# Optimization experiments

Hardware: AMD Instinct MI355X
Metric: run time of the kernel (lower is better)

Reference implementation:

```python
import jax, jax.numpy as jnp
import numpy as np

SCALES = (128.0, 256.0, 512.0)
ASPECT = (0.5, 1.0, 2.0)
K = 9
NMS_THR = 0.7
PRE_NMS_TOPK = 10000
POST_NMS_TOPK = 2000
MIN_SIZE = 16.0

def conv2d(x, w, b, pad):
    out = jax.lax.conv_general_dilated(x, w, (1, 1), [(pad, pad), (pad, pad)], dimension_numbers=('NCHW', 'OIHW', 'NCHW'))
    return out + b[None, :, None, None]

def generate_anchors(grid_h, grid_w, dtype):
    # Faithful to source: shifts are grid indices, NOT multiplied by stride (source bug kept).
    scales = jnp.asarray(SCALES, dtype)
    ar = jnp.asarray(ASPECT, dtype)
    h_ratio = jnp.sqrt(ar)
    w_ratio = 1.0 / h_ratio
    ws = (w_ratio[:, None] * scales[None, :]).reshape(-1)
    hs = (h_ratio[:, None] * scales[None, :]).reshape(-1)
    base = jnp.round(jnp.stack([-ws, -hs, ws, hs], axis=1) / 2.0)  # (9,4)
    sy, sx = jnp.meshgrid(jnp.arange(grid_h), jnp.arange(grid_w), indexing='ij')
    sx = sx.reshape(-1).astype(dtype)
    sy = sy.reshape(-1).astype(dtype)
    shifts = jnp.stack([sx, sy, sx, sy], axis=1)  # (H*W,4)
    return (shifts[:, None, :] + base[None, :, :]).reshape(-1, 4)  # (H*W*9,4)

def decode(box_pred, anchors):
    w = anchors[:, 2] - anchors[:, 0]
    h = anchors[:, 3] - anchors[:, 1]
    cx = anchors[:, 0] + 0.5 * w
    cy = anchors[:, 1] + 0.5 * h
    dx, dy, dw, dh = box_pred[:, 0], box_pred[:, 1], box_pred[:, 2], box_pred[:, 3]
    pcx = dx * w + cx
    pcy = dy * h + cy
    pw = jnp.exp(dw) * w
    ph = jnp.exp(dh) * h
    return jnp.stack([pcx - 0.5 * pw, pcy - 0.5 * ph, pcx + 0.5 * pw, pcy + 0.5 * ph], axis=1)

def nms_keep(boxes, valid, thr):
    # Greedy NMS on score-descending boxes; invalid (small) boxes never kept nor suppress others.
    n = boxes.shape[0]
    x1, y1, x2, y2 = boxes[:, 0], boxes[:, 1], boxes[:, 2], boxes[:, 3]
    areas = (x2 - x1) * (y2 - y1)
    idx = jnp.arange(n)
    def body(i, keep):
        xx1 = jnp.maximum(x1, x1[i]); yy1 = jnp.maximum(y1, y1[i])
        xx2 = jnp.minimum(x2, x2[i]); yy2 = jnp.minimum(y2, y2[i])
        inter = jnp.maximum(xx2 - xx1, 0.0) * jnp.maximum(yy2 - yy1, 0.0)
        iou = inter / (areas + areas[i] - inter)
        suppress = (iou > thr) & (idx > i) & keep[i]
        return keep & (~suppress)
    return jax.lax.fori_loop(0, n, body, valid)

def filter_proposals(proposals, cls_scores, img_h, img_w):
    scores = jax.nn.sigmoid(cls_scores.reshape(-1))
    top_scores, top_idx = jax.lax.top_k(scores, PRE_NMS_TOPK)  # sorted descending
    props = proposals[top_idx]
    x1 = jnp.clip(props[:, 0], 0.0, img_w); y1 = jnp.clip(props[:, 1], 0.0, img_h)
    x2 = jnp.clip(props[:, 2], 0.0, img_w); y2 = jnp.clip(props[:, 3], 0.0, img_h)
    props = jnp.stack([x1, y1, x2, y2], axis=1)
    valid = ((x2 - x1) >= MIN_SIZE) & ((y2 - y1) >= MIN_SIZE)
    keep = jax.lax.stop_gradient(nms_keep(jax.lax.stop_gradient(props), valid, NMS_THR))
    masked = jnp.where(keep, top_scores, -1.0)
    final_scores, final_idx = jax.lax.top_k(masked, POST_NMS_TOPK)  # order = score-descending (matches post-NMS sort)
    final_props = props[final_idx]
    valid_out = final_scores > 0.0  # sigmoid scores > 0, padding = -1
    return jnp.where(valid_out[:, None], final_props, 0.0), jnp.where(valid_out, final_scores, 0.0)

def setup_inputs():
    key = jax.random.key(0)
    ks = jax.random.split(key, 8)
    C = 512; GH = GW = 50
    feat = jax.random.normal(ks[0], (1, C, GH, GW), jnp.float32)
    image = jnp.zeros((1, 3, 800, 800), jnp.float32)
    gt_boxes = jax.random.uniform(ks[1], (8, 4), jnp.float32) * 800.0
    w_rpn = jax.random.normal(ks[2], (C, C, 3, 3), jnp.float32) * 0.01
    b_rpn = jnp.zeros((C,), jnp.float32)
    w_cls = jax.random.normal(ks[3], (K, C, 1, 1), jnp.float32) * 0.01
    b_cls = jnp.zeros((K,), jnp.float32)
    w_reg = jax.random.normal(ks[4], (4 * K, C, 1, 1), jnp.float32) * 0.01
    b_reg = jnp.zeros((4 * K,), jnp.float32)
    return {"image": image, "feat": feat, "gt_boxes": gt_boxes, "w_rpn": w_rpn, "b_rpn": b_rpn, "w_cls": w_cls, "b_cls": b_cls, "w_reg": w_reg, "b_reg": b_reg}

def reference(image, feat, gt_boxes, w_rpn, b_rpn, w_cls, b_cls, w_reg, b_reg):
    rpn_feat = jax.nn.relu(conv2d(feat, w_rpn, b_rpn, 1))
    cls = conv2d(rpn_feat, w_cls, b_cls, 0)      # (B,9,H,W)
    reg = conv2d(rpn_feat, w_reg, b_reg, 0)      # (B,36,H,W)
    B, _, gh, gw = feat.shape
    anchors = generate_anchors(gh, gw, feat.dtype)
    # flatten to anchor ordering (h, w, k) matching generate_anchors
    cls_flat = jnp.transpose(cls, (0, 2, 3, 1)).reshape(-1)
    reg_flat = jnp.transpose(reg.reshape(B, K, 4, gh, gw), (0, 3, 4, 1, 2)).reshape(-1, 4)
    proposals = decode(reg_flat, anchors)
    img_h, img_w = float(image.shape[-2]), float(image.shape[-1])
    return filter_proposals(proposals, cls_flat, img_h, img_w)
```

## Files before the change

### kernel.cpp

```cpp
#include <hip/hip_runtime.h>
#include <cmath>
#include <cstdint>
#include <cstddef>

typedef unsigned long long u64;
typedef unsigned int u32;

#define NPX   2500
#define NANCH 22500
#define PRE_TOPK 10000
#define NWORDS 160

struct AnchorBase { float b[36]; };

typedef __attribute__((ext_vector_type(8))) short bf16x8;
typedef __attribute__((ext_vector_type(4))) float f32x4;

__device__ inline unsigned short f2bf(float f) {
    u32 u = __float_as_uint(f);
    u32 r = u + 0x7fffu + ((u >> 16) & 1u);
    return (unsigned short)(r >> 16);
}
__device__ inline float bf2f(unsigned short h) {
    return __uint_as_float(((u32)h) << 16);
}

__global__ __launch_bounds__(256) void kprep(const float* __restrict__ feat,
                                             const float* __restrict__ wr,
                                             unsigned short* __restrict__ xthi,
                                             unsigned short* __restrict__ xtlo,
                                             unsigned short* __restrict__ whi,
                                             unsigned short* __restrict__ wlo)
{
    __shared__ float sh[4608];
    int bid = blockIdx.x;
    int t = threadIdx.x;
    if (bid < 416) {
        float (*tile)[65] = (float(*)[65])sh;
        int gr = bid >> 3;
        int cc = bid & 7;
        int tx = t & 63, ty = t >> 6;
        int y = gr - 1;
        bool rowok = (gr >= 1) && (gr <= 50);
#pragma unroll
        for (int i = 0; i < 16; ++i) {
            int c = i * 4 + ty;
            tile[c][tx] = (rowok && tx < 50)
                        ? feat[(size_t)(cc * 64 + c) * NPX + y * 50 + tx] : 0.f;
        }
        __syncthreads();
#pragma unroll
        for (int i = 0; i < 16; ++i) {
            int xp = i * 4 + ty;
            int cell = gr * 64 + xp;
            bool ok = rowok && xp >= 1 && xp <= 50;
            float v = ok ? tile[tx][xp - 1] : 0.f;
            unsigned short hi = f2bf(v);
            xthi[(size_t)cell * 512 + cc * 64 + tx] = hi;
            xtlo[(size_t)cell * 512 + cc * 64 + tx] = f2bf(v - bf2f(hi));
        }
    } else {
        int oc = bid - 416;
        for (int j = t; j < 4608; j += 256) sh[j] = wr[(size_t)oc * 4608 + j];
        __syncthreads();
        for (int k = t; k < 4608; k += 256) {
            int c = k & 511, tap = k >> 9;
            float v = sh[c * 9 + tap];
            unsigned short hi = f2bf(v);
            whi[(size_t)oc * 4608 + k] = hi;
            wlo[(size_t)oc * 4608 + k] = f2bf(v - bf2f(hi));
        }
    }
}

__global__ __launch_bounds__(256) void k1m(const unsigned short* __restrict__ xthi,
                                           const unsigned short* __restrict__ xtlo,
                                           const unsigned short* __restrict__ whi,
                                           const unsigned short* __restrict__ wlo,
                                           float* __restrict__ pk,
                                           int cptLog, int cptm1, int cptMul, int niter)
{
    __shared__ __align__(16) unsigned short Ah[8192];
    __shared__ __align__(16) unsigned short Al[8192];
    __shared__ __align__(16) unsigned short Bh[8192];
    __shared__ __align__(16) unsigned short Bl[8192];

    int t = threadIdx.x;
    int lane = t & 63, wave = t >> 6;
    int wo = wave & 1, wp = wave >> 1;
    int ocb = blockIdx.x, pxb = blockIdx.y, bs = blockIdx.z;
    int q = lane >> 4, m = lane & 15;
    int c0base = bs * cptMul;

    int g  = t & 7;
    int r0 = t >> 3;
    int cellB[4];
    int ocA[4];
#pragma unroll
    for (int i = 0; i < 4; ++i) {
        int rl = r0 + 32 * i;
        int opx = pxb * 128 + rl;
        cellB[i] = (opx < NPX) ? ((opx / 50) + 1) * 64 + (opx % 50) + 1 : 190;
        ocA[i] = ocb * 128 + rl;
    }

    f32x4 acc[16];
    f32x4 zf = {0.f, 0.f, 0.f, 0.f};
#pragma unroll
    for (int i = 0; i < 16; ++i) acc[i] = zf;

    for (int it = 0; it < niter; ++it) {
        int tap = it >> cptLog;
        int cw  = it & cptm1;
        int c0  = c0base + cw * 64;
        int t3  = (tap * 43) >> 7;
        int tapoff = (t3 - 1) * 64 + (tap - t3 * 3) - 1;
#pragma unroll
        for (int i = 0; i < 4; ++i) {
            int rl = r0 + 32 * i;
            int la = rl * 64 + g * 8;
            size_t ga = (size_t)ocA[i] * 4608 + tap * 512 + c0 + g * 8;
            *(bf16x8*)(Ah + la) = *(const bf16x8*)(whi + ga);
            *(bf16x8*)(Al + la) = *(const bf16x8*)(wlo + ga);
            size_t gb = (size_t)(cellB[i] + tapoff) * 512 + c0 + g * 8;
            *(bf16x8*)(Bh + la) = *(const bf16x8*)(xthi + gb);
            *(bf16x8*)(Bl + la) = *(const bf16x8*)(xtlo + gb);
        }
        __syncthreads();
#pragma unroll
        for (int ks = 0; ks < 2; ++ks) {
            bf16x8 fah[4], fal[4], fbh[4], fbl[4];
#pragma unroll
            for (int mt = 0; mt < 4; ++mt) {
                int off = (wo * 64 + mt * 16 + m) * 64 + ks * 32 + q * 8;
                fah[mt] = *(const bf16x8*)(Ah + off);
                fal[mt] = *(const bf16x8*)(Al + off);
            }
#pragma unroll
            for (int nt = 0; nt < 4; ++nt) {
                int off = (wp * 64 + nt * 16 + m) * 64 + ks * 32 + q * 8;
                fbh[nt] = *(const bf16x8*)(Bh + off);
                fbl[nt] = *(const bf16x8*)(Bl + off);
            }
#pragma unroll
            for (int mt = 0; mt < 4; ++mt)
#pragma unroll
                for (int nt = 0; nt < 4; ++nt) {
                    f32x4 a = acc[mt * 4 + nt];
                    a = __builtin_amdgcn_mfma_f32_16x16x32_bf16(fal[mt], fbh[nt], a, 0, 0, 0);
                    a = __builtin_amdgcn_mfma_f32_16x16x32_bf16(fah[mt], fbl[nt], a, 0, 0, 0);
                    a = __builtin_amdgcn_mfma_f32_16x16x32_bf16(fah[mt], fbh[nt], a, 0, 0, 0);
                    acc[mt * 4 + nt] = a;
                }
        }
        __syncthreads();
    }
#pragma unroll
    for (int mt = 0; mt < 4; ++mt)
#pragma unroll
        for (int nt = 0; nt < 4; ++nt)
#pragma unroll
            for (int r = 0; r < 4; ++r) {
                int oc = ocb * 128 + wo * 64 + mt * 16 + q * 4 + r;
                int px = pxb * 128 + wp * 64 + nt * 16 + m;
                pk[((size_t)bs * 512 + oc) * 2560 + px] = acc[mt * 4 + nt][r];
            }
}

__global__ __launch_bounds__(256) void k2a_heads(const float* __restrict__ pk, int ns,
                                                 const float* __restrict__ br,
                                                 const float* __restrict__ wcls,
                                                 const float* __restrict__ wreg,
                                                 float* __restrict__ part)
{
    __shared__ float vt[64 * 64];
    __shared__ float Wl[45 * 64];
    int t  = threadIdx.x;
    int pb = blockIdx.x;
    int s  = blockIdx.y;
    int cb = s * 64;
    for (int e = t; e < 45 * 64; e += 256) {
        int u = e >> 6, c = e & 63;
        Wl[e] = (u < 9) ? wcls[u * 512 + cb + c] : wreg[(u - 9) * 512 + cb + c];
    }
    int pxl = t & 63, ug = t >> 6;
    int px = pb * 64 + pxl;
    bool ok = px < NPX;
#pragma unroll
    for (int i = 0; i < 16; ++i) {
        int c = ug * 16 + i;
        float v = 0.f;
        if (ok) {
            size_t bidx = (size_t)(cb + c) * 2560 + px;
            v = br[cb + c];
            for (int ks = 0; ks < ns; ++ks) v += pk[(size_t)ks * 512 * 2560 + bidx];
            v = v > 0.f ? v : 0.f;
        }
        vt[c * 64 + pxl] = v;
    }
    __syncthreads();
    int ubase = ug * 12;
    int ulim  = (45 - ubase < 12) ? (45 - ubase) : 12;
    float acc[12];
#pragma unroll
    for (int j = 0; j < 12; ++j) acc[j] = 0.f;
    for (int c = 0; c < 64; ++c) {
        float v = vt[c * 64 + pxl];
#pragma unroll
        for (int j = 0; j < 12; ++j)
            acc[j] = fmaf(v, Wl[(ubase + j) * 64 + c], acc[j]);
    }
    if (ok) {
        for (int j = 0; j < ulim; ++j)
            part[((size_t)s * 45 + ubase + j) * NPX + px] = acc[j];
    }
}

__global__ __launch_bounds__(256) void k2b_decode(const float* __restrict__ part,
                                                  const float* __restrict__ bcls,
                                                  const float* __restrict__ breg,
                                                  AnchorBase ab,
                                                  float* __restrict__ score,
                                                  float* __restrict__ bx1, float* __restrict__ by1,
                                                  float* __restrict__ bx2, float* __restrict__ by2,
                                                  u32* __restrict__ valid,
                                                  u64* __restrict__ key)
{
    int id = blockIdx.x * 256 + threadIdx.x;
    if (id >= NANCH) return;
    int k  = id / NPX;
    int px = id - k * NPX;

    float z  = bcls[k];
    float d0 = breg[k * 4 + 0], d1 = breg[k * 4 + 1];
    float d2 = breg[k * 4 + 2], d3 = breg[k * 4 + 3];
#pragma unroll
    for (int s = 0; s < 8; ++s) {
        const float* p = part + (size_t)s * 45 * NPX;
        z  += p[(size_t)k * NPX + px];
        d0 += p[(size_t)(9 + k * 4 + 0) * NPX + px];
        d1 += p[(size_t)(9 + k * 4 + 1) * NPX + px];
        d2 += p[(size_t)(9 + k * 4 + 2) * NPX + px];
        d3 += p[(size_t)(9 + k * 4 + 3) * NPX + px];
    }
    float sc = 1.f / (1.f + expf(-z));

    int yy = px / 50, xx = px - (px / 50) * 50;
    float fx = (float)xx, fy = (float)yy;
    float ax1 = fx + ab.b[k * 4 + 0], ay1 = fy + ab.b[k * 4 + 1];
    float ax2 = fx + ab.b[k * 4 + 2], ay2 = fy + ab.b[k * 4 + 3];
    float aw = ax2 - ax1, ah = ay2 - ay1;
    float cx = ax1 + 0.5f * aw, cy = ay1 + 0.5f * ah;
    float pcx = d0 * aw + cx, pcy = d1 * ah + cy;
    float pw = expf(d2) * aw, ph = expf(d3) * ah;
    float x1 = pcx - 0.5f * pw, y1 = pcy - 0.5f * ph;
    float x2 = pcx + 0.5f * pw, y2 = pcy + 0.5f * ph;
    x1 = fminf(fmaxf(x1, 0.f), 800.f);
    y1 = fminf(fmaxf(y1, 0.f), 800.f);
    x2 = fminf(fmaxf(x2, 0.f), 800.f);
    y2 = fminf(fmaxf(y2, 0.f), 800.f);
    u32 v = ((x2 - x1) >= 16.f) && ((y2 - y1) >= 16.f);

    int f = px * 9 + k;
    score[f] = sc;
    bx1[f] = x1; by1[f] = y1; bx2[f] = x2; by2[f] = y2;
    valid[f] = v;
    u32 sb = __float_as_uint(sc);
    key[f] = ((u64)(~sb) << 32) | (u32)f;
}

__global__ __launch_bounds__(256) void k3a_rank(const u64* __restrict__ key,
                                                u32* __restrict__ rankp)
{
    __shared__ __align__(16) u64 sk[2250];
    int t  = threadIdx.x;
    int jb = blockIdx.y;
    for (int e = t; e < 2250; e += 256) sk[e] = key[jb * 2250 + e];
    __syncthreads();
    int i0 = blockIdx.x * 1024 + t;
    int i1 = i0 + 256, i2 = i0 + 512, i3 = i0 + 768;
    u64 k0 = (i0 < NANCH) ? key[i0] : 0ull;
    u64 k1 = (i1 < NANCH) ? key[i1] : 0ull;
    u64 k2 = (i2 < NANCH) ? key[i2] : 0ull;
    u64 k3 = (i3 < NANCH) ? key[i3] : 0ull;
    u32 c0 = 0, c1 = 0, c2 = 0, c3 = 0;
    const ulonglong2* sk2 = (const ulonglong2*)sk;
#pragma unroll 5
    for (int j = 0; j < 1125; ++j) {
        ulonglong2 v = sk2[j];
        c0 += (v.x < k0) ? 1u : 0u;  c0 += (v.y < k0) ? 1u : 0u;
        c1 += (v.x < k1) ? 1u : 0u;  c1 += (v.y < k1) ? 1u : 0u;
        c2 += (v.x < k2) ? 1u : 0u;  c2 += (v.y < k2) ? 1u : 0u;
        c3 += (v.x < k3) ? 1u : 0u;  c3 += (v.y < k3) ? 1u : 0u;
    }
    size_t base = (size_t)jb * NANCH;
    if (i0 < NANCH) rankp[base + i0] = c0;
    if (i1 < NANCH) rankp[base + i1] = c1;
    if (i2 < NANCH) rankp[base + i2] = c2;
    if (i3 < NANCH) rankp[base + i3] = c3;
}

__global__ __launch_bounds__(256) void k3b_gather(const u32* __restrict__ rankp,
                                                  const float* __restrict__ score,
                                                  const float* __restrict__ bx1, const float* __restrict__ by1,
                                                  const float* __restrict__ bx2, const float* __restrict__ by2,
                                                  const u32* __restrict__ valid,
                                                  float* __restrict__ sS,
                                                  float* __restrict__ sx1, float* __restrict__ sy1,
                                                  float* __restrict__ sx2, float* __restrict__ sy2,
                                                  float4* __restrict__ sbox4,
                                                  u32* __restrict__ sInv)
{
    int i = blockIdx.x * 256 + threadIdx.x;
    if (i >= NANCH) return;
    u32 r = 0;
#pragma unroll
    for (int c = 0; c < 10; ++c) r += rankp[(size_t)c * NANCH + i];
    if (r >= PRE_TOPK) return;
    float x1 = bx1[i], y1 = by1[i], x2 = bx2[i], y2 = by2[i];
    sS[r] = score[i];
    sx1[r] = x1; sy1[r] = y1; sx2[r] = x2; sy2[r] = y2;
    float4 b4; b4.x = x1; b4.y = y1; b4.z = x2; b4.w = y2;
    sbox4[r] = b4;
    sInv[r] = valid[i] ? 0u : 1u;
}

__global__ __launch_bounds__(256) void k4_mat(const float4* __restrict__ sbox4,
                                              u64* __restrict__ rows,
                                              u64* __restrict__ selfw)
{
    int t = threadIdx.x, lane = t & 63, wave = t >> 6;
    int i = blockIdx.x * 4 + wave;
    if (i >= PRE_TOPK) return;
    float4 bi = sbox4[i];
    float ai = (bi.z - bi.x) * (bi.w - bi.y);
    int wd  = i >> 6;
    int ish = i & 63;
    u64 diagmask = ~((2ull << ish) - 1ull);
    u64* rowp = rows + (size_t)i * NWORDS;
    for (int w = wd; w < 157; ++w) {
        float4 bj = sbox4[(w << 6) + lane];
        float xx1 = fmaxf(bi.x, bj.x);
        float yy1 = fmaxf(bi.y, bj.y);
        float xx2 = fminf(bi.z, bj.z);
        float yy2 = fminf(bi.w, bj.w);
        float iw = fmaxf(xx2 - xx1, 0.f);
        float ih = fmaxf(yy2 - yy1, 0.f);
        float inter = iw * ih;
        float aj = (bj.z - bj.x) * (bj.w - bj.y);
        float uni = ai + aj - inter;
        u64 b = __ballot(inter > 0.7f * uni);
        if (w == wd)  b &= diagmask;
        if (w == 156) b &= 0xFFFFull;
        if (lane == 0) {
            rowp[w] = b;
            if (w == wd) selfw[i] = b;
        }
    }
}

__global__ __launch_bounds__(64) void k5_scan(const u64* __restrict__ rows,
                                              const u64* __restrict__ selfw,
                                              const u32* __restrict__ sInv,
                                              const float* __restrict__ sS,
                                              const float* __restrict__ sx1, const float* __restrict__ sy1,
                                              const float* __restrict__ sx2, const float* __restrict__ sy2,
                                              float* __restrict__ out)
{
    __shared__ int keptList[2000];
    __shared__ int kcnt;
    int l = threadIdx.x;
    auto bw = [&](int w) -> u64 {
        const uint4* p = (const uint4*)(sInv + (size_t)w * 64);
        u64 v = 0;
#pragma unroll
        for (int j = 0; j < 16; ++j) {
            uint4 q = p[j];
            v |= ((u64)(q.x != 0) << (j * 4))     | ((u64)(q.y != 0) << (j * 4 + 1))
               | ((u64)(q.z != 0) << (j * 4 + 2)) | ((u64)(q.w != 0) << (j * 4 + 3));
        }
        return v;
    };
    u64 r0 = bw(l);
    u64 r1 = bw(64 + l);
    u64 r2 = (l < 32) ? bw(128 + l) : ~0ull;
    u64 swreg = selfw[l];
    int cnt = 0;
    bool done = false;
    for (int w = 0; w < 157 && !done; ++w) {
        u64 swnext = (w < 156) ? selfw[(size_t)(w + 1) * 64 + l] : 0ull;
        int slot = w >> 6, owner = w & 63;
        u64 val = (slot == 0) ? r0 : (slot == 1) ? r1 : r2;
        u64 rw = __shfl(val, owner, 64);
        u64 wmask = (w == 156) ? 0xFFFFull : ~0ull;
        u64 av = (~rw) & wmask;
        u64 km = 0;
        while (av) {
            int b = __ffsll((unsigned long long)av) - 1;
            u64 sw = __shfl(swreg, b, 64);
            km |= 1ull << b;
            av &= ~(1ull << b);
            av &= ~sw;
        }
        u64 kk = km;
        while (kk) {
            int bsx[16];
            int nb = 0;
            while (kk && nb < 16) {
                int b = __ffsll((unsigned long long)kk) - 1;
                kk &= kk - 1;
                bsx[nb++] = b;
            }
            u64 a0 = 0, a1 = 0, a2 = 0;
#pragma unroll
            for (int u = 0; u < 16; ++u) {
                if (u < nb) {
                    int i = (w << 6) + bsx[u];
                    if (l == 0 && cnt + u < 2000) keptList[cnt + u] = i;
                    const u64* rp = rows + (size_t)i * NWORDS;
                    a0 |= rp[l];
                    a1 |= rp[64 + l];
                    if (l < 32) a2 |= rp[128 + l];
                }
            }
            r0 |= a0; r1 |= a1; r2 |= a2;
            cnt += nb;
            if (cnt >= 2000) { done = true; break; }
        }
        swreg = swnext;
    }
    if (l == 0) kcnt = (cnt < 2000) ? cnt : 2000;
    __syncthreads();
    int K = kcnt;
    for (int r = l; r < 2000; r += 64) {
        if (r < K) {
            int j = keptList[r];
            out[r * 4 + 0] = sx1[j];
            out[r * 4 + 1] = sy1[j];
            out[r * 4 + 2] = sx2[j];
            out[r * 4 + 3] = sy2[j];
            out[8000 + r]  = sS[j];
        } else {
            out[r * 4 + 0] = 0.f; out[r * 4 + 1] = 0.f;
            out[r * 4 + 2] = 0.f; out[r * 4 + 3] = 0.f;
            out[8000 + r]  = 0.f;
        }
    }
}

extern "C" void kernel_launch(void* const* d_in, const int* in_sizes, int n_in,
                              void* d_out, int out_size, void* d_ws, size_t ws_size,
                              hipStream_t stream)
{
    (void)in_sizes; (void)n_in; (void)out_size;
    const float* feat = (const float*)d_in[1];
    const float* wrpn = (const float*)d_in[3];
    const float* brpn = (const float*)d_in[4];
    const float* wcls = (const float*)d_in[5];
    const float* bcls = (const float*)d_in[6];
    const float* wreg = (const float*)d_in[7];
    const float* breg = (const float*)d_in[8];
    float* out = (float*)d_out;

    int ns = (ws_size >= 58195968) ? 8 : (ws_size >= 37224448) ? 4 : 2;
    int cpt     = 8 / ns;
    int cptLog  = (ns == 2) ? 2 : (ns == 4) ? 1 : 0;
    int cptm1   = cpt - 1;
    int cptMul  = cpt * 64;
    int niter   = 9 * cpt;
    size_t pkB = (size_t)ns * 512 * 2560 * 4;

    char* ws = (char*)d_ws;
    float* pk = (float*)ws;
    unsigned short* Xthi = (unsigned short*)(ws + pkB);
    unsigned short* Xtlo = Xthi + (size_t)52 * 64 * 512;
    unsigned short* Whi  = (unsigned short*)(ws + pkB + 6815744);
    unsigned short* Wlo  = Whi + (size_t)512 * 4608;

    char* sm = ws + pkB;
    float* score = (float*)(sm + 0);
    float* bx1   = (float*)(sm + 90000);
    float* by1   = (float*)(sm + 180000);
    float* bx2   = (float*)(sm + 270000);
    float* by2   = (float*)(sm + 360000);
    u32*   valid = (u32*)  (sm + 450000);
    u64*   key   = (u64*)  (sm + 540000);
    u32*   rankp = (u32*)  (sm + 720000);
    float* sS    = (float*)(sm + 1620000);
    float* sx1   = (float*)(sm + 1660000);
    float* sy1   = (float*)(sm + 1700000);
    float* sx2   = (float*)(sm + 1740000);
    float* sy2   = (float*)(sm + 1780000);
    u32*   sInv  = (u32*)  (sm + 1820000);
    u64*   selfw = (u64*)  (sm + 1860960);
    float4* sbox4= (float4*)(sm + 1942880);
    float* part  = (float*)(sm + 2106720);
    u64*   rows  = (u64*)  (sm + 2106720);

    AnchorBase ab;
    {
        const float scales[3] = {128.f, 256.f, 512.f};
        const float aspect[3] = {0.5f, 1.f, 2.f};
        for (int ai = 0; ai < 3; ++ai) {
            float hr = sqrtf(aspect[ai]);
            float wratio = 1.0f / hr;
            for (int si = 0; si < 3; ++si) {
                float wsz = wratio * scales[si];
                float hsz = hr * scales[si];
                int a = ai * 3 + si;
                ab.b[a * 4 + 0] = rintf(-wsz / 2.0f);
                ab.b[a * 4 + 1] = rintf(-hsz / 2.0f);
                ab.b[a * 4 + 2] = rintf( wsz / 2.0f);
                ab.b[a * 4 + 3] = rintf( hsz / 2.0f);
            }
        }
    }

    kprep    <<<928, 256, 0, stream>>>(feat, wrpn, Xthi, Xtlo, Whi, Wlo);
    k1m      <<<dim3(4, 20, ns), 256, 0, stream>>>(Xthi, Xtlo, Whi, Wlo, pk,
                                                   cptLog, cptm1, cptMul, niter);
    k2a_heads<<<dim3(40, 8), 256, 0, stream>>>(pk, ns, brpn, wcls, wreg, part);
    k2b_decode<<<88, 256, 0, stream>>>(part, bcls, breg, ab, score, bx1, by1, bx2, by2, valid, key);
    k3a_rank <<<dim3(22, 10), 256, 0, stream>>>(key, rankp);
    k3b_gather<<<88, 256, 0, stream>>>(rankp, score, bx1, by1, bx2, by2, valid,
                                       sS, sx1, sy1, sx2, sy2, sbox4, sInv);
    hipMemsetAsync(rows, 0, (size_t)PRE_TOPK * NWORDS * 8, stream);
    k4_mat   <<<2500, 256, 0, stream>>>(sbox4, rows, selfw);
    k5_scan  <<<1, 64, 0, stream>>>(rows, selfw, sInv, sS, sx1, sy1, sx2, sy2, out);
}
```

Before: 384.6 us.

## Halve conv GEMM pixel tile and prefetch NMS self-masks in batches

The conv GEMM kernel's pixel tile shrinks from 128 to 64 per block, with the grid doubled in y. Each block now holds 8 accumulators instead of 16, and the B tile in LDS is halved. This gives more blocks for occupancy on the 256-CU part, at the cost of reloading the weight tiles twice as often. Separately, the serial NMS scan kernel now prefetches self-suppression words eight at a time, double-buffered, instead of one ahead, to hide global load latency in its single-wave loop.

```diff
diff --git a/kernel.cpp b/kernel.cpp
--- a/kernel.cpp
+++ b/kernel.cpp
@@ -82,8 +82,8 @@
 {
     __shared__ __align__(16) unsigned short Ah[8192];
     __shared__ __align__(16) unsigned short Al[8192];
-    __shared__ __align__(16) unsigned short Bh[8192];
-    __shared__ __align__(16) unsigned short Bl[8192];
+    __shared__ __align__(16) unsigned short Bh[4096];
+    __shared__ __align__(16) unsigned short Bl[4096];
 
     int t = threadIdx.x;
     int lane = t & 63, wave = t >> 6;
@@ -94,20 +94,20 @@
 
     int g  = t & 7;
     int r0 = t >> 3;
-    int cellB[4];
     int ocA[4];
-#pragma unroll
-    for (int i = 0; i < 4; ++i) {
-        int rl = r0 + 32 * i;
-        int opx = pxb * 128 + rl;
+    int cellB[2];
+#pragma unroll
+    for (int i = 0; i < 4; ++i) ocA[i] = ocb * 128 + r0 + 32 * i;
+#pragma unroll
+    for (int i = 0; i < 2; ++i) {
+        int opx = pxb * 64 + r0 + 32 * i;
         cellB[i] = (opx < NPX) ? ((opx / 50) + 1) * 64 + (opx % 50) + 1 : 190;
-        ocA[i] = ocb * 128 + rl;
-    }
-
-    f32x4 acc[16];
+    }
+
+    f32x4 acc[8];
     f32x4 zf = {0.f, 0.f, 0.f, 0.f};
 #pragma unroll
-    for (int i = 0; i < 16; ++i) acc[i] = zf;
+    for (int i = 0; i < 8; ++i) acc[i] = zf;
 
     for (int it = 0; it < niter; ++it) {
         int tap = it >> cptLog;
@@ -122,6 +122,11 @@
             size_t ga = (size_t)ocA[i] * 4608 + tap * 512 + c0 + g * 8;
             *(bf16x8*)(Ah + la) = *(const bf16x8*)(whi + ga);
             *(bf16x8*)(Al + la) = *(const bf16x8*)(wlo + ga);
+        }
+#pragma unroll
+        for (int i = 0; i < 2; ++i) {
+            int rl = r0 + 32 * i;
+            int la = rl * 64 + g * 8;
             size_t gb = (size_t)(cellB[i] + tapoff) * 512 + c0 + g * 8;
             *(bf16x8*)(Bh + la) = *(const bf16x8*)(xthi + gb);
             *(bf16x8*)(Bl + la) = *(const bf16x8*)(xtlo + gb);
@@ -129,7 +134,7 @@
         __syncthreads();
 #pragma unroll
         for (int ks = 0; ks < 2; ++ks) {
-            bf16x8 fah[4], fal[4], fbh[4], fbl[4];
+            bf16x8 fah[4], fal[4], fbh[2], fbl[2];
 #pragma unroll
             for (int mt = 0; mt < 4; ++mt) {
                 int off = (wo * 64 + mt * 16 + m) * 64 + ks * 32 + q * 8;
@@ -137,20 +142,20 @@
                 fal[mt] = *(const bf16x8*)(Al + off);
             }
 #pragma unroll
-            for (int nt = 0; nt < 4; ++nt) {
-                int off = (wp * 64 + nt * 16 + m) * 64 + ks * 32 + q * 8;
+            for (int nt = 0; nt < 2; ++nt) {
+                int off = (wp * 32 + nt * 16 + m) * 64 + ks * 32 + q * 8;
                 fbh[nt] = *(const bf16x8*)(Bh + off);
                 fbl[nt] = *(const bf16x8*)(Bl + off);
             }
 #pragma unroll
             for (int mt = 0; mt < 4; ++mt)
 #pragma unroll
-                for (int nt = 0; nt < 4; ++nt) {
-                    f32x4 a = acc[mt * 4 + nt];
+                for (int nt = 0; nt < 2; ++nt) {
+                    f32x4 a = acc[mt * 2 + nt];
                     a = __builtin_amdgcn_mfma_f32_16x16x32_bf16(fal[mt], fbh[nt], a, 0, 0, 0);
                     a = __builtin_amdgcn_mfma_f32_16x16x32_bf16(fah[mt], fbl[nt], a, 0, 0, 0);
                     a = __builtin_amdgcn_mfma_f32_16x16x32_bf16(fah[mt], fbh[nt], a, 0, 0, 0);
-                    acc[mt * 4 + nt] = a;
+                    acc[mt * 2 + nt] = a;
                 }
         }
         __syncthreads();
@@ -158,12 +163,12 @@
 #pragma unroll
     for (int mt = 0; mt < 4; ++mt)
 #pragma unroll
-        for (int nt = 0; nt < 4; ++nt)
+        for (int nt = 0; nt < 2; ++nt)
 #pragma unroll
             for (int r = 0; r < 4; ++r) {
                 int oc = ocb * 128 + wo * 64 + mt * 16 + q * 4 + r;
-                int px = pxb * 128 + wp * 64 + nt * 16 + m;
-                pk[((size_t)bs * 512 + oc) * 2560 + px] = acc[mt * 4 + nt][r];
+                int px = pxb * 64 + wp * 32 + nt * 16 + m;
+                pk[((size_t)bs * 512 + oc) * 2560 + px] = acc[mt * 2 + nt][r];
             }
 }
 
@@ -384,50 +389,73 @@
     u64 r0 = bw(l);
     u64 r1 = bw(64 + l);
     u64 r2 = (l < 32) ? bw(128 + l) : ~0ull;
-    u64 swreg = selfw[l];
+
+    u64 cur[8], nxt[8];
+#pragma unroll
+    for (int k = 0; k < 8; ++k) cur[k] = selfw[(size_t)k * 64 + l];
+#pragma unroll
+    for (int k = 0; k < 8; ++k) {
+        int ww = 8 + k;
+        nxt[k] = (ww < 157) ? selfw[(size_t)ww * 64 + l] : 0ull;
+    }
+
     int cnt = 0;
     bool done = false;
-    for (int w = 0; w < 157 && !done; ++w) {
-        u64 swnext = (w < 156) ? selfw[(size_t)(w + 1) * 64 + l] : 0ull;
-        int slot = w >> 6, owner = w & 63;
-        u64 val = (slot == 0) ? r0 : (slot == 1) ? r1 : r2;
-        u64 rw = __shfl(val, owner, 64);
-        u64 wmask = (w == 156) ? 0xFFFFull : ~0ull;
-        u64 av = (~rw) & wmask;
-        u64 km = 0;
-        while (av) {
-            int b = __ffsll((unsigned long long)av) - 1;
-            u64 sw = __shfl(swreg, b, 64);
-            km |= 1ull << b;
-            av &= ~(1ull << b);
-            av &= ~sw;
-        }
-        u64 kk = km;
-        while (kk) {
-            int bsx[16];
-            int nb = 0;
-            while (kk && nb < 16) {
-                int b = __ffsll((unsigned long long)kk) - 1;
-                kk &= kk - 1;
-                bsx[nb++] = b;
-            }
-            u64 a0 = 0, a1 = 0, a2 = 0;
-#pragma unroll
-            for (int u = 0; u < 16; ++u) {
-                if (u < nb) {
-                    int i = (w << 6) + bsx[u];
-                    if (l == 0 && cnt + u < 2000) keptList[cnt + u] = i;
-                    const u64* rp = rows + (size_t)i * NWORDS;
-                    a0 |= rp[l];
-                    a1 |= rp[64 + l];
-                    if (l < 32) a2 |= rp[128 + l];
+    for (int wg = 0; wg < 20; ++wg) {
+#pragma unroll
+        for (int ph = 0; ph < 8; ++ph) {
+            int w = wg * 8 + ph;
+            if (done || w > 156) continue;
+            u64 swreg = cur[ph];
+            int slot = w >> 6, owner = w & 63;
+            u64 val = (slot == 0) ? r0 : (slot == 1) ? r1 : r2;
+            u64 rw = __shfl(val, owner, 64);
+            u64 wmask = (w == 156) ? 0xFFFFull : ~0ull;
+            u64 av = (~rw) & wmask;
+            u64 km = 0;
+            while (av) {
+                int b = __ffsll((unsigned long long)av) - 1;
+                u64 sw = __shfl(swreg, b, 64);
+                km |= 1ull << b;
+                av &= ~(1ull << b);
+                av &= ~sw;
+            }
+            u64 kk = km;
+            while (kk) {
+                int bsx[16];
+                int nb = 0;
+                while (kk && nb < 16) {
+                    int b = __ffsll((unsigned long long)kk) - 1;
+                    kk &= kk - 1;
+                    bsx[nb++] = b;
                 }
-            }
-            r0 |= a0; r1 |= a1; r2 |= a2;
-            cnt += nb;
-            if (cnt >= 2000) { done = true; break; }
-        }
-        swreg = swnext;
+                u64 a0 = 0, a1 = 0, a2 = 0;
+#pragma unroll
+                for (int u = 0; u < 16; ++u) {
+                    if (u < nb) {
+                        int i = (w << 6) + bsx[u];
+                        if (l == 0 && cnt + u < 2000) keptList[cnt + u] = i;
+                        const u64* rp = rows + (size_t)i * NWORDS;
+                        a0 |= rp[l];
+                        a1 |= rp[64 + l];
+                        if (l < 32) a2 |= rp[128 + l];
+                    }
+                }
+                r0 |= a0; r1 |= a1; r2 |= a2;
+                cnt += nb;
+                if (cnt >= 2000) { done = true; break; }
+            }
+        }
+        if (!done) {
+            int base = (wg + 2) * 8;
+#pragma unroll
+            for (int k = 0; k < 8; ++k) cur[k] = nxt[k];
+#pragma unroll
+            for (int k = 0; k < 8; ++k) {
+                int ww = base + k;
+                nxt[k] = (ww < 157) ? selfw[(size_t)ww * 64 + l] : 0ull;
+            }
+        }
     }
     if (l == 0) kcnt = (cnt < 2000) ? cnt : 2000;
     __syncthreads();
@@ -517,7 +545,7 @@
     }
 
     kprep    <<<928, 256, 0, stream>>>(feat, wrpn, Xthi, Xtlo, Whi, Wlo);
-    k1m      <<<dim3(4, 20, ns), 256, 0, stream>>>(Xthi, Xtlo, Whi, Wlo, pk,
+    k1m      <<<dim3(4, 40, ns), 256, 0, stream>>>(Xthi, Xtlo, Whi, Wlo, pk,
                                                    cptLog, cptm1, cptMul, niter);
     k2a_heads<<<dim3(40, 8), 256, 0, stream>>>(pk, ns, brpn, wcls, wreg, part);
     k2b_decode<<<88, 256, 0, stream>>>(part, bcls, breg, ab, score, bx1, by1, bx2, by2, valid, key);
```

New measurement: 371.7 us. 1.03x faster.
